# Kernel optimization log

Hardware: AMD Instinct MI355X
Metric: run time of the kernel (lower is better)

Reference implementation:

```python
import jax, jax.numpy as jnp
import numpy as np

Z_DIM, Y_DIM, X_DIM, N_ACT = 32, 16, 64, 4
TINY_H, HEAD_H = 64, 32
INNER_STEPS, SUP_STEPS = 2, 2
BATCH = 524288


def setup_inputs() -> dict:
    key = jax.random.key(0)
    ks = jax.random.split(key, 12)
    s = lambda k, shp, fan_in: jax.random.normal(k, shp, jnp.float32) * (1.0 / np.sqrt(fan_in))
    return {
        "state": jax.random.normal(ks[0], (BATCH, X_DIM), jnp.float32),
        "prev_action": jax.random.randint(ks[1], (BATCH, 1), 0, N_ACT, jnp.int64),
        "z0": jax.random.normal(ks[2], (1, 1, Z_DIM), jnp.float32) * 0.1,
        # TinyNetwork: Linear(112 -> 64), Linear(64 -> 32); weights stored [out, in]
        "Wt1": s(ks[3], (TINY_H, Z_DIM + X_DIM + Y_DIM), Z_DIM + X_DIM + Y_DIM),
        "bt1": jnp.zeros((TINY_H,), jnp.float32),
        "Wt2": s(ks[4], (Z_DIM, TINY_H), TINY_H),
        "bt2": jnp.zeros((Z_DIM,), jnp.float32),
        # OutputHead: Linear(48 -> 32), Linear(32 -> 4)
        "Wh1": s(ks[5], (HEAD_H, Z_DIM + Y_DIM), Z_DIM + Y_DIM),
        "bh1": jnp.zeros((HEAD_H,), jnp.float32),
        "Wh2": s(ks[6], (N_ACT, HEAD_H), HEAD_H),
        "bh2": jnp.zeros((N_ACT,), jnp.float32),
        # action embedding table [n_actions, y_dim]
        "emb": jax.random.normal(ks[7], (N_ACT, Y_DIM), jnp.float32),
    }


def reference(state, prev_action, z0, Wt1, bt1, Wt2, bt2, Wh1, bh1, Wh2, bh2, emb):
    B = state.shape[0]
    x = state[:, None, :]                      # [B, 1, x_dim]
    y = emb[prev_action]                       # [B, 1, y_dim]
    z = jnp.broadcast_to(z0, (B, 1, Z_DIM))    # [B, 1, z_dim]

    def tiny(z, x, y):
        inp = jnp.concatenate([z, x, y], axis=-1)           # [B,1,112]
        h = jax.nn.relu(inp @ Wt1.T + bt1)                  # [B,1,64]
        return h @ Wt2.T + bt2                              # [B,1,32]

    def head(z, y):
        inp = jnp.concatenate([z, y], axis=-1)              # [B,1,48]
        h = jax.nn.relu(inp @ Wh1.T + bh1)                  # [B,1,32]
        return h @ Wh2.T + bh2                              # [B,1,4]

    logits = None
    for _ in range(SUP_STEPS):
        for _ in range(INNER_STEPS):
            z = tiny(z, x, y)
        logits = head(z, y)
        probs = jax.nn.softmax(logits, axis=-1)             # [B,1,4]
        y = probs @ emb                                     # [B,1,16]
    return logits[:, 0, :]                                  # squeeze seq dim
```

## Files before the change

### kernel.cpp

```cpp
#include <hip/hip_runtime.h>
#include <hip/hip_bf16.h>

typedef __attribute__((ext_vector_type(8))) short bf16x8;
typedef __attribute__((ext_vector_type(4))) float f32x4;

#define MFMA16(A,B,C) __builtin_amdgcn_mfma_f32_16x16x32_bf16((A),(B),(C),0,0,0)

static __device__ __forceinline__ f32x4 ld4(const float* p){
  return *(const f32x4*)p;
}
static __device__ __forceinline__ unsigned pk2(float a, float b){
  unsigned r;
  asm("v_cvt_pk_bf16_f32 %0, %1, %2" : "=v"(r) : "v"(a), "v"(b));
  return r;
}
static __device__ __forceinline__ bf16x8 mk8(float a,float b,float c,float d,
                                             float e,float f,float g,float h){
  union { bf16x8 v; unsigned u[4]; } r;
  r.u[0]=pk2(a,b); r.u[1]=pk2(c,d); r.u[2]=pk2(e,f); r.u[3]=pk2(g,h);
  return r.v;
}
static __device__ __forceinline__ bf16x8 mk8v(f32x4 a, f32x4 b){
  return mk8(a[0],a[1],a[2],a[3],b[0],b[1],b[2],b[3]);
}
static __device__ __forceinline__ bf16x8 mk8r(f32x4 a, f32x4 b){
  return mk8(fmaxf(a[0],0.f),fmaxf(a[1],0.f),fmaxf(a[2],0.f),fmaxf(a[3],0.f),
             fmaxf(b[0],0.f),fmaxf(b[1],0.f),fmaxf(b[2],0.f),fmaxf(b[3],0.f));
}
static __device__ __forceinline__ bf16x8 zero8(){
  bf16x8 v;
  #pragma unroll
  for(int i=0;i<8;++i) v[i]=0;
  return v;
}
static __device__ __forceinline__ bf16x8 one8(){
  bf16x8 v = zero8();
  v[0] = (short)0x3F80;
  return v;
}
static __device__ __forceinline__ void keepa(bf16x8& v){ asm("" : "+a"(v)); }
static __device__ __forceinline__ void keepaf(f32x4& v){ asm("" : "+a"(v)); }
static __device__ __forceinline__ void keepv(bf16x8& v){ asm("" : "+v"(v)); }
static __device__ __forceinline__ void keepvf(f32x4& v){ asm("" : "+v"(v)); }

__global__ __launch_bounds__(256, 2) void trm_mfma(
    const float* __restrict__ state, const int* __restrict__ pact,
    const float* __restrict__ z0,
    const float* __restrict__ Wt1, const float* __restrict__ bt1,
    const float* __restrict__ Wt2, const float* __restrict__ bt2,
    const float* __restrict__ Wh1, const float* __restrict__ bh1,
    const float* __restrict__ Wh2, const float* __restrict__ bh2,
    const float* __restrict__ emb, float* __restrict__ out,
    int ntiles, int wstride)
{
  __shared__ __align__(16) float ef[64];
  const int lane = threadIdx.x & 63;
  const int wid  = blockIdx.x * (blockDim.x >> 6) + (threadIdx.x >> 6);
  const int r16  = lane & 15;
  const int hi   = lane >> 4;
  const int he   = hi & 1;

  if (threadIdx.x < 64) ef[threadIdx.x] = emb[threadIdx.x];
  __syncthreads();

  f32x4 b2[8];
  #pragma unroll
  for (int q=0;q<8;++q) b2[q] = ld4(bt2 + q*4);
  float bt1p[4];
  #pragma unroll
  for (int m=0;m<4;++m){
    const float* w = Wt1 + (m*16 + r16)*112;
    f32x4 s = b2[0]*ld4(w);
    #pragma unroll
    for (int q=1;q<8;++q) s += b2[q]*ld4(w + q*4);
    bt1p[m] = bt1[m*16 + r16] + s[0]+s[1]+s[2]+s[3];
  }
  float bh1p[2];
  #pragma unroll
  for (int m=0;m<2;++m){
    const float* w = Wh1 + (m*16 + r16)*48;
    f32x4 s = b2[0]*ld4(w);
    #pragma unroll
    for (int q=1;q<8;++q) s += b2[q]*ld4(w + q*4);
    bh1p[m] = bh1[m*16 + r16] + s[0]+s[1]+s[2]+s[3];
  }

  bf16x8 wt1f[4][4];
  #pragma unroll
  for (int m=0;m<4;++m){
    const float* w = Wt1 + (m*16 + r16)*112;
    wt1f[m][0] = mk8v(ld4(w + hi*4),       ld4(w + 16 + hi*4));
    wt1f[m][1] = mk8v(ld4(w + 32 + hi*8),  ld4(w + 36 + hi*8));
    wt1f[m][2] = mk8v(ld4(w + 64 + hi*8),  ld4(w + 68 + hi*8));
    bf16x8 yfrag;
    if (hi < 2)       yfrag = mk8v(ld4(w + 96 + hi*8), ld4(w + 100 + hi*8));
    else if (hi == 2) yfrag = mk8(bt1p[m],0.f,0.f,0.f,0.f,0.f,0.f,0.f);
    else              yfrag = zero8();
    wt1f[m][3] = yfrag;
    keepa(wt1f[m][0]); keepa(wt1f[m][1]); keepa(wt1f[m][2]); keepa(wt1f[m][3]);
  }
  bf16x8 wt2f[2][2];
  #pragma unroll
  for (int m=0;m<2;++m){
    const float* w = Wt2 + (m*16 + r16)*64;
    wt2f[m][0] = mk8v(ld4(w + hi*4),      ld4(w + 16 + hi*4));
    wt2f[m][1] = mk8v(ld4(w + 32 + hi*4), ld4(w + 48 + hi*4));
    keepa(wt2f[m][0]); keepa(wt2f[m][1]);
  }
  bf16x8 wh1f[2][2];
  #pragma unroll
  for (int m=0;m<2;++m){
    const float* w = Wh1 + (m*16 + r16)*48;
    wh1f[m][0] = mk8v(ld4(w + hi*4), ld4(w + 16 + hi*4));
    bf16x8 yfrag;
    if (hi < 2)       yfrag = mk8v(ld4(w + 32 + hi*8), ld4(w + 36 + hi*8));
    else if (hi == 2) yfrag = mk8(bh1p[m],0.f,0.f,0.f,0.f,0.f,0.f,0.f);
    else              yfrag = zero8();
    wh1f[m][1] = yfrag;
    keepa(wh1f[m][0]); keepa(wh1f[m][1]);
  }
  bf16x8 wh2f;
  {
    const float* w = Wh2 + ((r16 < 4) ? r16 : 0)*32;
    bf16x8 t = mk8v(ld4(w + hi*4), ld4(w + 16 + hi*4));
    if (r16 >= 4) t = zero8();
    wh2f = t;
    keepa(wh2f);
  }
  f32x4 bh2r;
  {
    f32x4 t = ld4(bh2);
    float msk = (hi == 0) ? 1.f : 0.f;
    bh2r = t * msk;
    keepaf(bh2r);
  }
  f32x4 zero4 = {0.f, 0.f, 0.f, 0.f};
  keepvf(zero4);
  bf16x8 z0f;
  {
    f32x4 za = ld4(z0 + hi*4)      - ld4(bt2 + hi*4);
    f32x4 zb = ld4(z0 + 16 + hi*4) - ld4(bt2 + 16 + hi*4);
    z0f = mk8v(za, zb);
    keepv(z0f);
  }

  int t = wid;
  f32x4 cx0, cx1, cx2, cx3; int cact;
  {
    const int col = t*16 + r16;
    const float* xr = state + (size_t)col*64;
    cx0 = ld4(xr + hi*8);      cx1 = ld4(xr + hi*8 + 4);
    cx2 = ld4(xr + 32 + hi*8); cx3 = ld4(xr + 36 + hi*8);
    cact = pact[col];
  }

  #pragma unroll 1
  for (; t < ntiles; t += wstride){
    const int col = t*16 + r16;
    bf16x8 xf0 = mk8v(cx0, cx1);
    bf16x8 xf1 = mk8v(cx2, cx3);
    bf16x8 yf;
    {
      const float* er = ef + cact*16 + he*8;
      yf = mk8v(ld4(er), ld4(er + 4));
      if (hi == 2) yf = one8();
      if (hi == 3) yf = zero8();
    }

    const int tn = t + wstride;
    if (tn < ntiles){
      const int coln = tn*16 + r16;
      const float* xrn = state + (size_t)coln*64;
      cx0 = ld4(xrn + hi*8);      cx1 = ld4(xrn + hi*8 + 4);
      cx2 = ld4(xrn + 32 + hi*8); cx3 = ld4(xrn + 36 + hi*8);
      cact = pact[coln];
    }

    bf16x8 zf = z0f;
    f32x4 lgv;

    #pragma unroll
    for (int s=0;s<2;++s){
      #pragma unroll
      for (int itr=0; itr<2; ++itr){
        f32x4 c0 = MFMA16(wt1f[0][0], zf, zero4);
        f32x4 c1 = MFMA16(wt1f[1][0], zf, zero4);
        f32x4 c2 = MFMA16(wt1f[2][0], zf, zero4);
        f32x4 c3 = MFMA16(wt1f[3][0], zf, zero4);
        c0=MFMA16(wt1f[0][1], xf0, c0); c1=MFMA16(wt1f[1][1], xf0, c1);
        c2=MFMA16(wt1f[2][1], xf0, c2); c3=MFMA16(wt1f[3][1], xf0, c3);
        c0=MFMA16(wt1f[0][2], xf1, c0); c1=MFMA16(wt1f[1][2], xf1, c1);
        c2=MFMA16(wt1f[2][2], xf1, c2); c3=MFMA16(wt1f[3][2], xf1, c3);
        c0=MFMA16(wt1f[0][3], yf,  c0); c1=MFMA16(wt1f[1][3], yf,  c1);
        c2=MFMA16(wt1f[2][3], yf,  c2); c3=MFMA16(wt1f[3][3], yf,  c3);
        bf16x8 h0 = mk8r(c0, c1);
        bf16x8 h1 = mk8r(c2, c3);
        f32x4 d0 = MFMA16(wt2f[0][0], h0, zero4);
        f32x4 d1 = MFMA16(wt2f[1][0], h0, zero4);
        d0=MFMA16(wt2f[0][1], h1, d0);
        d1=MFMA16(wt2f[1][1], h1, d1);
        zf = mk8v(d0, d1);
      }
      f32x4 g0 = MFMA16(wh1f[0][0], zf, zero4);
      f32x4 g1 = MFMA16(wh1f[1][0], zf, zero4);
      g0=MFMA16(wh1f[0][1], yf, g0);
      g1=MFMA16(wh1f[1][1], yf, g1);
      bf16x8 hh = mk8r(g0, g1);
      f32x4 cl = MFMA16(wh2f, hh, bh2r);
      lgv = cl;
      if (s == 0){
        float l0 = __shfl(cl[0], r16), l1 = __shfl(cl[1], r16);
        float l2 = __shfl(cl[2], r16), l3 = __shfl(cl[3], r16);
        float mx = fmaxf(fmaxf(l0,l1), fmaxf(l2,l3));
        float p0=__expf(l0-mx), p1=__expf(l1-mx);
        float p2=__expf(l2-mx), p3=__expf(l3-mx);
        float inv = 1.f/(p0+p1+p2+p3);
        p0*=inv; p1*=inv; p2*=inv; p3*=inv;
        const float* eb = ef + he*8;
        f32x4 ya = ld4(eb)*p0      + ld4(eb+16)*p1 +
                   ld4(eb+32)*p2   + ld4(eb+48)*p3;
        f32x4 yb = ld4(eb+4)*p0    + ld4(eb+20)*p1 +
                   ld4(eb+36)*p2   + ld4(eb+52)*p3;
        yf = mk8v(ya, yb);
        if (hi == 2) yf = one8();
        if (hi == 3) yf = zero8();
      }
    }
    if (hi == 0) *(f32x4*)(out + (size_t)col*4) = lgv;
  }
}

extern "C" void kernel_launch(void* const* d_in, const int* in_sizes, int n_in,
                              void* d_out, int out_size, void* d_ws, size_t ws_size,
                              hipStream_t stream) {
  const float* state = (const float*)d_in[0];
  const int*   pact  = (const int*)  d_in[1];
  const float* z0    = (const float*)d_in[2];
  const float* Wt1   = (const float*)d_in[3];
  const float* bt1   = (const float*)d_in[4];
  const float* Wt2   = (const float*)d_in[5];
  const float* bt2   = (const float*)d_in[6];
  const float* Wh1   = (const float*)d_in[7];
  const float* bh1   = (const float*)d_in[8];
  const float* Wh2   = (const float*)d_in[9];
  const float* bh2   = (const float*)d_in[10];
  const float* emb   = (const float*)d_in[11];
  float* out = (float*)d_out;

  const int B = in_sizes[0] / 64;
  const int ntiles = B / 16;
  const int blocks = 512;
  const int wstride = blocks * 4;
  trm_mfma<<<blocks, 256, 0, stream>>>(state, pact, z0, Wt1, bt1, Wt2, bt2,
                                       Wh1, bh1, Wh2, bh2, emb, out,
                                       ntiles, wstride);
}
```

Before: 64.59 us.

## Process two 16-column tiles per wave iteration with interleaved MFMA chains

Each wave now handles two independent 16-row tiles per loop iteration and interleaves their MFMA chains, so the dependent MFMA sequences of one tile can hide the latency of the other. The software prefetch of the next tile's state and actions is removed; loads are issued at the top of each iteration instead. This raises register pressure and doubles per-iteration work, and could lose the global-load latency hiding the prefetch gave.

```diff
diff --git a/kernel.cpp b/kernel.cpp
--- a/kernel.cpp
+++ b/kernel.cpp
@@ -51,7 +51,7 @@
     const float* __restrict__ Wh1, const float* __restrict__ bh1,
     const float* __restrict__ Wh2, const float* __restrict__ bh2,
     const float* __restrict__ emb, float* __restrict__ out,
-    int ntiles, int wstride)
+    int niters, int wstride)
 {
   __shared__ __align__(16) float ef[64];
   const int lane = threadIdx.x & 63;
@@ -130,8 +130,7 @@
   f32x4 bh2r;
   {
     f32x4 t = ld4(bh2);
-    float msk = (hi == 0) ? 1.f : 0.f;
-    bh2r = t * msk;
+    bh2r = t * ((hi == 0) ? 1.f : 0.f);
     keepaf(bh2r);
   }
   f32x4 zero4 = {0.f, 0.f, 0.f, 0.f};
@@ -144,89 +143,120 @@
     keepv(z0f);
   }
 
-  int t = wid;
-  f32x4 cx0, cx1, cx2, cx3; int cact;
-  {
-    const int col = t*16 + r16;
-    const float* xr = state + (size_t)col*64;
-    cx0 = ld4(xr + hi*8);      cx1 = ld4(xr + hi*8 + 4);
-    cx2 = ld4(xr + 32 + hi*8); cx3 = ld4(xr + 36 + hi*8);
-    cact = pact[col];
-  }
-
   #pragma unroll 1
-  for (; t < ntiles; t += wstride){
-    const int col = t*16 + r16;
-    bf16x8 xf0 = mk8v(cx0, cx1);
-    bf16x8 xf1 = mk8v(cx2, cx3);
-    bf16x8 yf;
+  for (int it = wid; it < niters; it += wstride){
+    const int colA = it*32 + r16, colB = colA + 16;
+    const float* xa = state + (size_t)colA*64;
+    const float* xb = state + (size_t)colB*64;
+    f32x4 ra0 = ld4(xa + hi*8),      ra1 = ld4(xa + hi*8 + 4);
+    f32x4 ra2 = ld4(xa + 32 + hi*8), ra3 = ld4(xa + 36 + hi*8);
+    f32x4 rb0 = ld4(xb + hi*8),      rb1 = ld4(xb + hi*8 + 4);
+    f32x4 rb2 = ld4(xb + 32 + hi*8), rb3 = ld4(xb + 36 + hi*8);
+    const int aA = pact[colA], aB = pact[colB];
+
+    bf16x8 xfA0 = mk8v(ra0, ra1), xfA1 = mk8v(ra2, ra3);
+    bf16x8 xfB0 = mk8v(rb0, rb1), xfB1 = mk8v(rb2, rb3);
+    bf16x8 yfA, yfB;
     {
-      const float* er = ef + cact*16 + he*8;
-      yf = mk8v(ld4(er), ld4(er + 4));
-      if (hi == 2) yf = one8();
-      if (hi == 3) yf = zero8();
-    }
-
-    const int tn = t + wstride;
-    if (tn < ntiles){
-      const int coln = tn*16 + r16;
-      const float* xrn = state + (size_t)coln*64;
-      cx0 = ld4(xrn + hi*8);      cx1 = ld4(xrn + hi*8 + 4);
-      cx2 = ld4(xrn + 32 + hi*8); cx3 = ld4(xrn + 36 + hi*8);
-      cact = pact[coln];
-    }
-
-    bf16x8 zf = z0f;
-    f32x4 lgv;
+      const float* er = ef + aA*16 + he*8;
+      yfA = mk8v(ld4(er), ld4(er + 4));
+      if (hi == 2) yfA = one8();
+      if (hi == 3) yfA = zero8();
+    }
+    {
+      const float* er = ef + aB*16 + he*8;
+      yfB = mk8v(ld4(er), ld4(er + 4));
+      if (hi == 2) yfB = one8();
+      if (hi == 3) yfB = zero8();
+    }
+    bf16x8 zfA = z0f, zfB = z0f;
+    f32x4 lgvA, lgvB;
 
     #pragma unroll
-    for (int s=0;s<2;++s){
+    for (int s = 0; s < 2; ++s){
       #pragma unroll
-      for (int itr=0; itr<2; ++itr){
-        f32x4 c0 = MFMA16(wt1f[0][0], zf, zero4);
-        f32x4 c1 = MFMA16(wt1f[1][0], zf, zero4);
-        f32x4 c2 = MFMA16(wt1f[2][0], zf, zero4);
-        f32x4 c3 = MFMA16(wt1f[3][0], zf, zero4);
-        c0=MFMA16(wt1f[0][1], xf0, c0); c1=MFMA16(wt1f[1][1], xf0, c1);
-        c2=MFMA16(wt1f[2][1], xf0, c2); c3=MFMA16(wt1f[3][1], xf0, c3);
-        c0=MFMA16(wt1f[0][2], xf1, c0); c1=MFMA16(wt1f[1][2], xf1, c1);
-        c2=MFMA16(wt1f[2][2], xf1, c2); c3=MFMA16(wt1f[3][2], xf1, c3);
-        c0=MFMA16(wt1f[0][3], yf,  c0); c1=MFMA16(wt1f[1][3], yf,  c1);
-        c2=MFMA16(wt1f[2][3], yf,  c2); c3=MFMA16(wt1f[3][3], yf,  c3);
-        bf16x8 h0 = mk8r(c0, c1);
-        bf16x8 h1 = mk8r(c2, c3);
-        f32x4 d0 = MFMA16(wt2f[0][0], h0, zero4);
-        f32x4 d1 = MFMA16(wt2f[1][0], h0, zero4);
-        d0=MFMA16(wt2f[0][1], h1, d0);
-        d1=MFMA16(wt2f[1][1], h1, d1);
-        zf = mk8v(d0, d1);
+      for (int itr = 0; itr < 2; ++itr){
+        f32x4 cA0 = MFMA16(wt1f[0][0], zfA, zero4);
+        f32x4 cB0 = MFMA16(wt1f[0][0], zfB, zero4);
+        f32x4 cA1 = MFMA16(wt1f[1][0], zfA, zero4);
+        f32x4 cB1 = MFMA16(wt1f[1][0], zfB, zero4);
+        f32x4 cA2 = MFMA16(wt1f[2][0], zfA, zero4);
+        f32x4 cB2 = MFMA16(wt1f[2][0], zfB, zero4);
+        f32x4 cA3 = MFMA16(wt1f[3][0], zfA, zero4);
+        f32x4 cB3 = MFMA16(wt1f[3][0], zfB, zero4);
+        cA0=MFMA16(wt1f[0][1], xfA0, cA0); cB0=MFMA16(wt1f[0][1], xfB0, cB0);
+        cA1=MFMA16(wt1f[1][1], xfA0, cA1); cB1=MFMA16(wt1f[1][1], xfB0, cB1);
+        cA2=MFMA16(wt1f[2][1], xfA0, cA2); cB2=MFMA16(wt1f[2][1], xfB0, cB2);
+        cA3=MFMA16(wt1f[3][1], xfA0, cA3); cB3=MFMA16(wt1f[3][1], xfB0, cB3);
+        cA0=MFMA16(wt1f[0][2], xfA1, cA0); cB0=MFMA16(wt1f[0][2], xfB1, cB0);
+        cA1=MFMA16(wt1f[1][2], xfA1, cA1); cB1=MFMA16(wt1f[1][2], xfB1, cB1);
+        cA2=MFMA16(wt1f[2][2], xfA1, cA2); cB2=MFMA16(wt1f[2][2], xfB1, cB2);
+        cA3=MFMA16(wt1f[3][2], xfA1, cA3); cB3=MFMA16(wt1f[3][2], xfB1, cB3);
+        cA0=MFMA16(wt1f[0][3], yfA, cA0);  cB0=MFMA16(wt1f[0][3], yfB, cB0);
+        cA1=MFMA16(wt1f[1][3], yfA, cA1);  cB1=MFMA16(wt1f[1][3], yfB, cB1);
+        cA2=MFMA16(wt1f[2][3], yfA, cA2);  cB2=MFMA16(wt1f[2][3], yfB, cB2);
+        cA3=MFMA16(wt1f[3][3], yfA, cA3);  cB3=MFMA16(wt1f[3][3], yfB, cB3);
+        bf16x8 hA0 = mk8r(cA0, cA1), hA1 = mk8r(cA2, cA3);
+        bf16x8 hB0 = mk8r(cB0, cB1), hB1 = mk8r(cB2, cB3);
+        f32x4 dA0 = MFMA16(wt2f[0][0], hA0, zero4);
+        f32x4 dB0 = MFMA16(wt2f[0][0], hB0, zero4);
+        f32x4 dA1 = MFMA16(wt2f[1][0], hA0, zero4);
+        f32x4 dB1 = MFMA16(wt2f[1][0], hB0, zero4);
+        dA0=MFMA16(wt2f[0][1], hA1, dA0); dB0=MFMA16(wt2f[0][1], hB1, dB0);
+        dA1=MFMA16(wt2f[1][1], hA1, dA1); dB1=MFMA16(wt2f[1][1], hB1, dB1);
+        zfA = mk8v(dA0, dA1); zfB = mk8v(dB0, dB1);
       }
-      f32x4 g0 = MFMA16(wh1f[0][0], zf, zero4);
-      f32x4 g1 = MFMA16(wh1f[1][0], zf, zero4);
-      g0=MFMA16(wh1f[0][1], yf, g0);
-      g1=MFMA16(wh1f[1][1], yf, g1);
-      bf16x8 hh = mk8r(g0, g1);
-      f32x4 cl = MFMA16(wh2f, hh, bh2r);
-      lgv = cl;
+      f32x4 gA0 = MFMA16(wh1f[0][0], zfA, zero4);
+      f32x4 gB0 = MFMA16(wh1f[0][0], zfB, zero4);
+      f32x4 gA1 = MFMA16(wh1f[1][0], zfA, zero4);
+      f32x4 gB1 = MFMA16(wh1f[1][0], zfB, zero4);
+      gA0=MFMA16(wh1f[0][1], yfA, gA0); gB0=MFMA16(wh1f[0][1], yfB, gB0);
+      gA1=MFMA16(wh1f[1][1], yfA, gA1); gB1=MFMA16(wh1f[1][1], yfB, gB1);
+      bf16x8 hhA = mk8r(gA0, gA1), hhB = mk8r(gB0, gB1);
+      f32x4 clA = MFMA16(wh2f, hhA, bh2r);
+      f32x4 clB = MFMA16(wh2f, hhB, bh2r);
+      lgvA = clA; lgvB = clB;
       if (s == 0){
-        float l0 = __shfl(cl[0], r16), l1 = __shfl(cl[1], r16);
-        float l2 = __shfl(cl[2], r16), l3 = __shfl(cl[3], r16);
-        float mx = fmaxf(fmaxf(l0,l1), fmaxf(l2,l3));
-        float p0=__expf(l0-mx), p1=__expf(l1-mx);
-        float p2=__expf(l2-mx), p3=__expf(l3-mx);
-        float inv = 1.f/(p0+p1+p2+p3);
-        p0*=inv; p1*=inv; p2*=inv; p3*=inv;
-        const float* eb = ef + he*8;
-        f32x4 ya = ld4(eb)*p0      + ld4(eb+16)*p1 +
-                   ld4(eb+32)*p2   + ld4(eb+48)*p3;
-        f32x4 yb = ld4(eb+4)*p0    + ld4(eb+20)*p1 +
-                   ld4(eb+36)*p2   + ld4(eb+52)*p3;
-        yf = mk8v(ya, yb);
-        if (hi == 2) yf = one8();
-        if (hi == 3) yf = zero8();
+        {
+          float l0=__shfl(clA[0],r16), l1=__shfl(clA[1],r16);
+          float l2=__shfl(clA[2],r16), l3=__shfl(clA[3],r16);
+          float mx = fmaxf(fmaxf(l0,l1), fmaxf(l2,l3));
+          float p0=__expf(l0-mx), p1=__expf(l1-mx);
+          float p2=__expf(l2-mx), p3=__expf(l3-mx);
+          float inv = 1.f/(p0+p1+p2+p3);
+          p0*=inv; p1*=inv; p2*=inv; p3*=inv;
+          const float* eb = ef + he*8;
+          f32x4 ya = ld4(eb)*p0    + ld4(eb+16)*p1 +
+                     ld4(eb+32)*p2 + ld4(eb+48)*p3;
+          f32x4 yb = ld4(eb+4)*p0  + ld4(eb+20)*p1 +
+                     ld4(eb+36)*p2 + ld4(eb+52)*p3;
+          yfA = mk8v(ya, yb);
+          if (hi == 2) yfA = one8();
+          if (hi == 3) yfA = zero8();
+        }
+        {
+          float l0=__shfl(clB[0],r16), l1=__shfl(clB[1],r16);
+          float l2=__shfl(clB[2],r16), l3=__shfl(clB[3],r16);
+          float mx = fmaxf(fmaxf(l0,l1), fmaxf(l2,l3));
+          float p0=__expf(l0-mx), p1=__expf(l1-mx);
+          float p2=__expf(l2-mx), p3=__expf(l3-mx);
+          float inv = 1.f/(p0+p1+p2+p3);
+          p0*=inv; p1*=inv; p2*=inv; p3*=inv;
+          const float* eb = ef + he*8;
+          f32x4 ya = ld4(eb)*p0    + ld4(eb+16)*p1 +
+                     ld4(eb+32)*p2 + ld4(eb+48)*p3;
+          f32x4 yb = ld4(eb+4)*p0  + ld4(eb+20)*p1 +
+                     ld4(eb+36)*p2 + ld4(eb+52)*p3;
+          yfB = mk8v(ya, yb);
+          if (hi == 2) yfB = one8();
+          if (hi == 3) yfB = zero8();
+        }
       }
     }
-    if (hi == 0) *(f32x4*)(out + (size_t)col*4) = lgv;
+    if (hi == 0){
+      *(f32x4*)(out + (size_t)colA*4) = lgvA;
+      *(f32x4*)(out + (size_t)colB*4) = lgvB;
+    }
   }
 }
 
@@ -248,10 +278,10 @@
   float* out = (float*)d_out;
 
   const int B = in_sizes[0] / 64;
-  const int ntiles = B / 16;
+  const int niters = B / 32;
   const int blocks = 512;
   const int wstride = blocks * 4;
   trm_mfma<<<blocks, 256, 0, stream>>>(state, pact, z0, Wt1, bt1, Wt2, bt2,
                                        Wh1, bh1, Wh2, bh2, emb, out,
-                                       ntiles, wstride);
-}
+                                       niters, wstride);
+}
```

Measured after the change: 69.81 us. 8.1% more time.

## Move Wt1 MFMA fragments to LDS to raise occupancy to 3 blocks/CU

Applied to the files above, without the earlier changes.

The 16 Wt1 bf16 fragments, previously held in AGPRs per thread, are now built once per block by the first wave into shared memory and re-read from LDS in every inner MFMA step. This frees register pressure so launch bounds can rise to 3 blocks per CU, and the grid grows from 512 to 768 blocks. The aim is more waves in flight to hide the global state loads. In exchange, each tiny-network step issues 16 LDS reads (16 KB per block), which may add latency into the MFMA chain.

```diff
diff --git a/kernel.cpp b/kernel.cpp
--- a/kernel.cpp
+++ b/kernel.cpp
@@ -43,7 +43,7 @@
 static __device__ __forceinline__ void keepv(bf16x8& v){ asm("" : "+v"(v)); }
 static __device__ __forceinline__ void keepvf(f32x4& v){ asm("" : "+v"(v)); }
 
-__global__ __launch_bounds__(256, 2) void trm_mfma(
+__global__ __launch_bounds__(256, 3) void trm_mfma(
     const float* __restrict__ state, const int* __restrict__ pact,
     const float* __restrict__ z0,
     const float* __restrict__ Wt1, const float* __restrict__ bt1,
@@ -53,6 +53,7 @@
     const float* __restrict__ emb, float* __restrict__ out,
     int ntiles, int wstride)
 {
+  __shared__ __align__(16) bf16x8 wlds[16*64];
   __shared__ __align__(16) float ef[64];
   const int lane = threadIdx.x & 63;
   const int wid  = blockIdx.x * (blockDim.x >> 6) + (threadIdx.x >> 6);
@@ -60,9 +61,6 @@
   const int hi   = lane >> 4;
   const int he   = hi & 1;
 
-  if (threadIdx.x < 64) ef[threadIdx.x] = emb[threadIdx.x];
-  __syncthreads();
-
   f32x4 b2[8];
   #pragma unroll
   for (int q=0;q<8;++q) b2[q] = ld4(bt2 + q*4);
@@ -85,20 +83,25 @@
     bh1p[m] = bh1[m*16 + r16] + s[0]+s[1]+s[2]+s[3];
   }
 
-  bf16x8 wt1f[4][4];
-  #pragma unroll
-  for (int m=0;m<4;++m){
-    const float* w = Wt1 + (m*16 + r16)*112;
-    wt1f[m][0] = mk8v(ld4(w + hi*4),       ld4(w + 16 + hi*4));
-    wt1f[m][1] = mk8v(ld4(w + 32 + hi*8),  ld4(w + 36 + hi*8));
-    wt1f[m][2] = mk8v(ld4(w + 64 + hi*8),  ld4(w + 68 + hi*8));
-    bf16x8 yfrag;
-    if (hi < 2)       yfrag = mk8v(ld4(w + 96 + hi*8), ld4(w + 100 + hi*8));
-    else if (hi == 2) yfrag = mk8(bt1p[m],0.f,0.f,0.f,0.f,0.f,0.f,0.f);
-    else              yfrag = zero8();
-    wt1f[m][3] = yfrag;
-    keepa(wt1f[m][0]); keepa(wt1f[m][1]); keepa(wt1f[m][2]); keepa(wt1f[m][3]);
-  }
+  if (threadIdx.x < 64){
+    ef[threadIdx.x] = emb[threadIdx.x];
+    #pragma unroll
+    for (int m=0;m<4;++m){
+      const float* w = Wt1 + (m*16 + r16)*112;
+      bf16x8 f0 = mk8v(ld4(w + hi*4),       ld4(w + 16 + hi*4));
+      bf16x8 f1 = mk8v(ld4(w + 32 + hi*8),  ld4(w + 36 + hi*8));
+      bf16x8 f2 = mk8v(ld4(w + 64 + hi*8),  ld4(w + 68 + hi*8));
+      bf16x8 f3;
+      if (hi < 2)       f3 = mk8v(ld4(w + 96 + hi*8), ld4(w + 100 + hi*8));
+      else if (hi == 2) f3 = mk8(bt1p[m],0.f,0.f,0.f,0.f,0.f,0.f,0.f);
+      else              f3 = zero8();
+      wlds[(m*4+0)*64 + lane] = f0;
+      wlds[(m*4+1)*64 + lane] = f1;
+      wlds[(m*4+2)*64 + lane] = f2;
+      wlds[(m*4+3)*64 + lane] = f3;
+    }
+  }
+
   bf16x8 wt2f[2][2];
   #pragma unroll
   for (int m=0;m<2;++m){
@@ -130,8 +133,7 @@
   f32x4 bh2r;
   {
     f32x4 t = ld4(bh2);
-    float msk = (hi == 0) ? 1.f : 0.f;
-    bh2r = t * msk;
+    bh2r = t * ((hi == 0) ? 1.f : 0.f);
     keepaf(bh2r);
   }
   f32x4 zero4 = {0.f, 0.f, 0.f, 0.f};
@@ -143,6 +145,7 @@
     z0f = mk8v(za, zb);
     keepv(z0f);
   }
+  __syncthreads();
 
   int t = wid;
   f32x4 cx0, cx1, cx2, cx3; int cact;
@@ -183,28 +186,37 @@
     for (int s=0;s<2;++s){
       #pragma unroll
       for (int itr=0; itr<2; ++itr){
-        f32x4 c0 = MFMA16(wt1f[0][0], zf, zero4);
-        f32x4 c1 = MFMA16(wt1f[1][0], zf, zero4);
-        f32x4 c2 = MFMA16(wt1f[2][0], zf, zero4);
-        f32x4 c3 = MFMA16(wt1f[3][0], zf, zero4);
-        c0=MFMA16(wt1f[0][1], xf0, c0); c1=MFMA16(wt1f[1][1], xf0, c1);
-        c2=MFMA16(wt1f[2][1], xf0, c2); c3=MFMA16(wt1f[3][1], xf0, c3);
-        c0=MFMA16(wt1f[0][2], xf1, c0); c1=MFMA16(wt1f[1][2], xf1, c1);
-        c2=MFMA16(wt1f[2][2], xf1, c2); c3=MFMA16(wt1f[3][2], xf1, c3);
-        c0=MFMA16(wt1f[0][3], yf,  c0); c1=MFMA16(wt1f[1][3], yf,  c1);
-        c2=MFMA16(wt1f[2][3], yf,  c2); c3=MFMA16(wt1f[3][3], yf,  c3);
+        bf16x8 a0, a1, a2, a3;
+        a0 = wlds[0*64+lane]; a1 = wlds[4*64+lane];
+        a2 = wlds[8*64+lane]; a3 = wlds[12*64+lane];
+        f32x4 c0 = MFMA16(a0, zf, zero4);
+        f32x4 c1 = MFMA16(a1, zf, zero4);
+        f32x4 c2 = MFMA16(a2, zf, zero4);
+        f32x4 c3 = MFMA16(a3, zf, zero4);
+        a0 = wlds[1*64+lane]; a1 = wlds[5*64+lane];
+        a2 = wlds[9*64+lane]; a3 = wlds[13*64+lane];
+        c0 = MFMA16(a0, xf0, c0); c1 = MFMA16(a1, xf0, c1);
+        c2 = MFMA16(a2, xf0, c2); c3 = MFMA16(a3, xf0, c3);
+        a0 = wlds[2*64+lane]; a1 = wlds[6*64+lane];
+        a2 = wlds[10*64+lane]; a3 = wlds[14*64+lane];
+        c0 = MFMA16(a0, xf1, c0); c1 = MFMA16(a1, xf1, c1);
+        c2 = MFMA16(a2, xf1, c2); c3 = MFMA16(a3, xf1, c3);
+        a0 = wlds[3*64+lane]; a1 = wlds[7*64+lane];
+        a2 = wlds[11*64+lane]; a3 = wlds[15*64+lane];
+        c0 = MFMA16(a0, yf, c0); c1 = MFMA16(a1, yf, c1);
+        c2 = MFMA16(a2, yf, c2); c3 = MFMA16(a3, yf, c3);
         bf16x8 h0 = mk8r(c0, c1);
         bf16x8 h1 = mk8r(c2, c3);
         f32x4 d0 = MFMA16(wt2f[0][0], h0, zero4);
         f32x4 d1 = MFMA16(wt2f[1][0], h0, zero4);
-        d0=MFMA16(wt2f[0][1], h1, d0);
-        d1=MFMA16(wt2f[1][1], h1, d1);
+        d0 = MFMA16(wt2f[0][1], h1, d0);
+        d1 = MFMA16(wt2f[1][1], h1, d1);
         zf = mk8v(d0, d1);
       }
       f32x4 g0 = MFMA16(wh1f[0][0], zf, zero4);
       f32x4 g1 = MFMA16(wh1f[1][0], zf, zero4);
-      g0=MFMA16(wh1f[0][1], yf, g0);
-      g1=MFMA16(wh1f[1][1], yf, g1);
+      g0 = MFMA16(wh1f[0][1], yf, g0);
+      g1 = MFMA16(wh1f[1][1], yf, g1);
       bf16x8 hh = mk8r(g0, g1);
       f32x4 cl = MFMA16(wh2f, hh, bh2r);
       lgv = cl;
@@ -249,7 +261,7 @@
 
   const int B = in_sizes[0] / 64;
   const int ntiles = B / 16;
-  const int blocks = 512;
+  const int blocks = 768;
   const int wstride = blocks * 4;
   trm_mfma<<<blocks, 256, 0, stream>>>(state, pact, z0, Wt1, bt1, Wt2, bt2,
                                        Wh1, bh1, Wh2, bh2, emb, out,
```

Result: slower. 81.31 us (+25.9%).
